# Optimization experiments

Measured on AMD Instinct MI355X. Metric: run time of the kernel, lower is better.

## Reference

```python
import jax, jax.numpy as jnp
import numpy as np

B, S, H, L, NH, FF, V, NL = 16, 512, 768, 12, 12, 3072, 30522, 9
DH = H // NH


def setup_inputs() -> dict:
    key = jax.random.key(0)
    ks = iter(jax.random.split(key, 16))
    def w(shape, scale=0.02):
        return jax.random.normal(next(ks), shape, jnp.float32) * scale
    return {
        "input_word_ids": jax.random.randint(next(ks), (B, S), 0, V, jnp.int32),
        "input_mask": jnp.ones((B, S), jnp.int32),
        "input_type_ids": jnp.zeros((B, S), jnp.int32),
        "valid_mask": jax.random.randint(next(ks), (B, S), 0, 2, jnp.int32),
        "word_emb": w((V, H)),
        "pos_emb": w((S, H)),
        "type_emb": w((2, H)),
        "emb_ln_g": jnp.ones((H,), jnp.float32),
        "emb_ln_b": jnp.zeros((H,), jnp.float32),
        "Wq": w((L, H, H)), "bq": jnp.zeros((L, H), jnp.float32),
        "Wk": w((L, H, H)), "bk": jnp.zeros((L, H), jnp.float32),
        "Wv": w((L, H, H)), "bv": jnp.zeros((L, H), jnp.float32),
        "Wo": w((L, H, H)), "bo": jnp.zeros((L, H), jnp.float32),
        "ln1_g": jnp.ones((L, H), jnp.float32), "ln1_b": jnp.zeros((L, H), jnp.float32),
        "W1": w((L, H, FF)), "b1": jnp.zeros((L, FF), jnp.float32),
        "W2": w((L, FF, H)), "b2": jnp.zeros((L, H), jnp.float32),
        "ln2_g": jnp.ones((L, H), jnp.float32), "ln2_b": jnp.zeros((L, H), jnp.float32),
        "cls_W": w((H, NL)), "cls_b": jnp.zeros((NL,), jnp.float32),
    }


def _layer_norm(x, g, b):
    m = x.mean(-1, keepdims=True)
    v = ((x - m) ** 2).mean(-1, keepdims=True)
    return (x - m) * jax.lax.rsqrt(v + 1e-12) * g + b


def reference(input_word_ids, input_mask, input_type_ids, valid_mask,
              word_emb, pos_emb, type_emb, emb_ln_g, emb_ln_b,
              Wq, bq, Wk, bk, Wv, bv, Wo, bo, ln1_g, ln1_b,
              W1, b1, W2, b2, ln2_g, ln2_b, cls_W, cls_b):
    b, s = input_word_ids.shape
    # --- BERT embeddings ---
    x = word_emb[input_word_ids] + pos_emb[None, :s] + type_emb[input_type_ids]
    x = _layer_norm(x, emb_ln_g, emb_ln_b)  # [B,S,H]
    attn_bias = (1.0 - input_mask.astype(jnp.float32))[:, None, None, :] * -1e9
    scale = 1.0 / np.sqrt(DH).astype(np.float32)

    def step(h, p):
        wq, bq_, wk, bk_, wv, bv_, wo, bo_, g1, gb1, w1, wb1, w2, wb2, g2, gb2 = p
        q = (h @ wq + bq_).reshape(b, s, NH, DH)
        k = (h @ wk + bk_).reshape(b, s, NH, DH)
        v = (h @ wv + bv_).reshape(b, s, NH, DH)
        scores = jnp.einsum('bqhd,bkhd->bhqk', q, k) * scale + attn_bias
        probs = jax.nn.softmax(scores, axis=-1)
        ctx = jnp.einsum('bhqk,bkhd->bqhd', probs, v).reshape(b, s, H)
        h = _layer_norm(h + ctx @ wo + bo_, g1, gb1)
        ff = jax.nn.gelu(h @ w1 + wb1, approximate=False)
        h = _layer_norm(h + ff @ w2 + wb2, g2, gb2)
        return h, None

    params = (Wq, bq, Wk, bk, Wv, bv, Wo, bo, ln1_g, ln1_b, W1, b1, W2, b2, ln2_g, ln2_b)
    x, _ = jax.lax.scan(step, x, params)

    # --- valid-token compaction (vectorized form of the python double loop) ---
    # valid tokens packed to the front (stable order), remainder zero-padded
    invalid = (1 - valid_mask).astype(jnp.int32)
    perm = jnp.argsort(invalid, axis=1, stable=True)          # [B,S]
    compact = jnp.take_along_axis(x, perm[:, :, None], axis=1)
    counts = valid_mask.sum(axis=1)                           # [B]
    keep = (jnp.arange(s)[None, :] < counts[:, None])[:, :, None]
    compact = jnp.where(keep, compact, jnp.zeros((), x.dtype))
    # dropout is identity at inference (training=False)
    logits = jax.nn.softmax(compact @ cls_W + cls_b, axis=-1)  # [B,S,NL]
    return logits
```

## Files before the change

### kernel.cpp

```cpp
#include <hip/hip_runtime.h>
#include <cstdint>
#include <cstddef>

#define B_ 16
#define S_ 512
#define H_ 768
#define L_ 12
#define NH_ 12
#define DH_ 64
#define FF_ 3072
#define NL_ 9
#define QKV_ 2304

typedef _Float16 f16x8 __attribute__((ext_vector_type(8)));
typedef float f32x4 __attribute__((ext_vector_type(4)));

__device__ __forceinline__ void load_lds16(const void* g, void* l) {
  __builtin_amdgcn_global_load_lds(
      (const __attribute__((address_space(1))) unsigned int*)g,
      (__attribute__((address_space(3))) unsigned int*)l, 16, 0, 0);
}

__device__ __forceinline__ float block_sum256(float v, float* red) {
#pragma unroll
  for (int off = 32; off; off >>= 1) v += __shfl_down(v, off);
  __syncthreads();
  if ((threadIdx.x & 63) == 0) red[threadIdx.x >> 6] = v;
  __syncthreads();
  return red[0] + red[1] + red[2] + red[3];
}

__device__ __forceinline__ float gelu_f(float x) {
  return 0.5f * x * (1.0f + erff(x * 0.70710678118654752f));
}

__global__ __launch_bounds__(256) void embed_ln_kernel(
    const int* __restrict__ wid, const int* __restrict__ tpid,
    const float* __restrict__ we, const float* __restrict__ pe,
    const float* __restrict__ te, const float* __restrict__ g,
    const float* __restrict__ bb, float* __restrict__ h,
    _Float16* __restrict__ hb) {
  __shared__ float red[4];
  int tok = blockIdx.x;
  int s = tok & (S_ - 1);
  int w = wid[tok], tp = tpid[tok];
  int t = threadIdx.x;
  float x[3];
#pragma unroll
  for (int i = 0; i < 3; ++i) {
    int j = t + i * 256;
    x[i] = we[(size_t)w * H_ + j] + pe[(size_t)s * H_ + j] + te[(size_t)tp * H_ + j];
  }
  float m = block_sum256(x[0] + x[1] + x[2], red) * (1.0f / H_);
  float d0 = x[0] - m, d1 = x[1] - m, d2 = x[2] - m;
  float var = block_sum256(d0 * d0 + d1 * d1 + d2 * d2, red) * (1.0f / H_);
  float rs = rsqrtf(var + 1e-12f);
#pragma unroll
  for (int i = 0; i < 3; ++i) {
    int j = t + i * 256;
    float v = (x[i] - m) * rs * g[j] + bb[j];
    h[(size_t)tok * H_ + j] = v;
    hb[(size_t)tok * H_ + j] = (_Float16)v;
  }
}

__global__ __launch_bounds__(256) void add_ln_kernel(
    float* __restrict__ h, const float* __restrict__ delta,
    const float* __restrict__ g, const float* __restrict__ bb,
    _Float16* __restrict__ hb) {
  __shared__ float red[4];
  int tok = blockIdx.x;
  int t = threadIdx.x;
  float x[3];
#pragma unroll
  for (int i = 0; i < 3; ++i) {
    int j = t + i * 256;
    x[i] = h[(size_t)tok * H_ + j] + delta[(size_t)tok * H_ + j];
  }
  float m = block_sum256(x[0] + x[1] + x[2], red) * (1.0f / H_);
  float d0 = x[0] - m, d1 = x[1] - m, d2 = x[2] - m;
  float var = block_sum256(d0 * d0 + d1 * d1 + d2 * d2, red) * (1.0f / H_);
  float rs = rsqrtf(var + 1e-12f);
#pragma unroll
  for (int i = 0; i < 3; ++i) {
    int j = t + i * 256;
    float v = (x[i] - m) * rs * g[j] + bb[j];
    h[(size_t)tok * H_ + j] = v;
    hb[(size_t)tok * H_ + j] = (_Float16)v;
  }
}

__global__ __launch_bounds__(256) void convert_weights_kernel(
    const float* __restrict__ Wq, const float* __restrict__ Wk,
    const float* __restrict__ Wv, const float* __restrict__ Wo,
    const float* __restrict__ W1, const float* __restrict__ W2,
    _Float16* __restrict__ qT, _Float16* __restrict__ kT,
    _Float16* __restrict__ vT, _Float16* __restrict__ oT,
    _Float16* __restrict__ w1T, _Float16* __restrict__ w2T,
    const float* __restrict__ bq, const float* __restrict__ bk,
    const float* __restrict__ bv, float* __restrict__ qkvb) {
  int id = blockIdx.x;
  int tid = threadIdx.x;
  if (id == 1728) {
    for (int j = tid; j < H_; j += 256) {
      qkvb[j] = bq[j];
      qkvb[H_ + j] = bk[j];
      qkvb[2 * H_ + j] = bv[j];
    }
    return;
  }
  __shared__ float T[64][65];
  const float* src;
  _Float16* dst;
  int K, N, tk, tn;
  if (id < 576) {
    int mat = id / 144, t = id % 144;
    K = 768; N = 768; tk = t / 12; tn = t % 12;
    src = (mat == 0) ? Wq : (mat == 1) ? Wk : (mat == 2) ? Wv : Wo;
    dst = (mat == 0) ? qT : (mat == 1) ? kT : (mat == 2) ? vT : oT;
  } else if (id < 1152) {
    int t = id - 576; K = 768; N = 3072; tk = t / 48; tn = t % 48;
    src = W1; dst = w1T;
  } else {
    int t = id - 1152; K = 3072; N = 768; tk = t / 12; tn = t % 12;
    src = W2; dst = w2T;
  }
  int k0 = tk * 64, n0 = tn * 64;
  {
    int r = tid >> 4, c4 = (tid & 15) * 4;
#pragma unroll
    for (int i = 0; i < 4; ++i) {
      float4 v = *(const float4*)&src[(size_t)(k0 + r + i * 16) * N + n0 + c4];
      T[r + i * 16][c4 + 0] = v.x;
      T[r + i * 16][c4 + 1] = v.y;
      T[r + i * 16][c4 + 2] = v.z;
      T[r + i * 16][c4 + 3] = v.w;
    }
  }
  __syncthreads();
#pragma unroll
  for (int i = 0; i < 2; ++i) {
    int chunk = tid + i * 256;
    int n = chunk >> 3, kc = (chunk & 7) * 8;
    f16x8 o;
#pragma unroll
    for (int j = 0; j < 8; ++j) o[j] = (_Float16)T[kc + j][n];
    *(f16x8*)&dst[(size_t)(n0 + n) * K + k0 + kc] = o;
  }
}

template <int OUT>
__global__ __launch_bounds__(256) void gemm_f16(
    const _Float16* __restrict__ A, const _Float16* __restrict__ Bt,
    const float* __restrict__ bias, void* __restrict__ Cv,
    int M, int N, int K) {
  __shared__ _Float16 As[2][128 * 32];
  __shared__ _Float16 Bs[2][128 * 32];
  int tid = threadIdx.x;
  int lane = tid & 63, w = tid >> 6;
  int wr = w >> 1, wc = w & 1;
  int l15 = lane & 15, kb = lane >> 4;
  int swk = (l15 >> 1) & 3;

  int nwg = gridDim.x * gridDim.y;
  int bid = blockIdx.y * gridDim.x + blockIdx.x;
  int swz = bid;
  if ((nwg & 7) == 0) {
    int cpx = nwg >> 3;
    swz = (bid & 7) * cpx + (bid >> 3);
  }
  int bx = swz % gridDim.x, by = swz / gridDim.x;
  int row0 = by * 128, col0 = bx * 128;

  int srow = lane >> 2;
  int schunk = (lane & 3) ^ ((lane >> 3) & 3);
  int scol = schunk * 8;
  const _Float16* gA0 = A + (size_t)(row0 + (w * 2 + 0) * 16 + srow) * K + scol;
  const _Float16* gA1 = A + (size_t)(row0 + (w * 2 + 1) * 16 + srow) * K + scol;
  const _Float16* gB0 = Bt + (size_t)(col0 + (w * 2 + 0) * 16 + srow) * K + scol;
  const _Float16* gB1 = Bt + (size_t)(col0 + (w * 2 + 1) * 16 + srow) * K + scol;
  int o0 = (w * 2 + 0) * 1024;
  int o1 = (w * 2 + 1) * 1024;

  f32x4 acc[4][4] = {};
  int nk = K >> 5;

  load_lds16(gA0, (char*)&As[0][0] + o0);
  load_lds16(gA1, (char*)&As[0][0] + o1);
  load_lds16(gB0, (char*)&Bs[0][0] + o0);
  load_lds16(gB1, (char*)&Bs[0][0] + o1);
  __syncthreads();

  for (int kt = 0; kt < nk; ++kt) {
    int cur = kt & 1;
    if (kt + 1 < nk) {
      int ko = (kt + 1) * 32;
      load_lds16(gA0 + ko, (char*)&As[cur ^ 1][0] + o0);
      load_lds16(gA1 + ko, (char*)&As[cur ^ 1][0] + o1);
      load_lds16(gB0 + ko, (char*)&Bs[cur ^ 1][0] + o0);
      load_lds16(gB1 + ko, (char*)&Bs[cur ^ 1][0] + o1);
    }
    f16x8 af[4], bf[4];
    int rpos = (kb ^ swk) * 8;
#pragma unroll
    for (int m = 0; m < 4; ++m)
      af[m] = *(const f16x8*)&As[cur][(wr * 64 + m * 16 + l15) * 32 + rpos];
#pragma unroll
    for (int n = 0; n < 4; ++n)
      bf[n] = *(const f16x8*)&Bs[cur][(wc * 64 + n * 16 + l15) * 32 + rpos];
#pragma unroll
    for (int m = 0; m < 4; ++m)
#pragma unroll
      for (int n = 0; n < 4; ++n)
        acc[m][n] = __builtin_amdgcn_mfma_f32_16x16x32_f16(af[m], bf[n], acc[m][n], 0, 0, 0);
    __syncthreads();
  }
#pragma unroll
  for (int n = 0; n < 4; ++n) {
    int col = col0 + wc * 64 + n * 16 + l15;
    float bv = bias[col];
#pragma unroll
    for (int m = 0; m < 4; ++m) {
      int rowb = row0 + wr * 64 + m * 16 + kb * 4;
#pragma unroll
      for (int r = 0; r < 4; ++r) {
        float v = acc[m][n][r] + bv;
        if (OUT == 2) v = gelu_f(v);
        if (OUT == 0)
          ((float*)Cv)[(size_t)(rowb + r) * N + col] = v;
        else
          ((_Float16*)Cv)[(size_t)(rowb + r) * N + col] = (_Float16)v;
      }
    }
  }
}

__global__ __launch_bounds__(256) void vtrans_kernel(
    const _Float16* __restrict__ v, int RS, _Float16* __restrict__ vt) {
  __shared__ _Float16 T[64][72];
  int s0 = blockIdx.x * 64;
  int bh = blockIdx.y;
  int b = bh / NH_, h = bh % NH_;
  int tid = threadIdx.x;
#pragma unroll
  for (int i = 0; i < 2; ++i) {
    int chunk = tid + i * 256;
    int s = chunk >> 3, dc = (chunk & 7) * 8;
    *(f16x8*)&T[s][dc] = *(const f16x8*)&v[(size_t)(b * S_ + s0 + s) * RS + h * DH_ + dc];
  }
  __syncthreads();
#pragma unroll
  for (int i = 0; i < 2; ++i) {
    int chunk = tid + i * 256;
    int d = chunk >> 3, sc = (chunk & 7) * 8;
    f16x8 o;
#pragma unroll
    for (int j = 0; j < 8; ++j) o[j] = T[sc + j][d];
    *(f16x8*)&vt[(size_t)(bh * DH_ + d) * S_ + s0 + sc] = o;
  }
}

__global__ __launch_bounds__(256) void flash_attn_kernel(
    const _Float16* __restrict__ q, const _Float16* __restrict__ k,
    const _Float16* __restrict__ vt, int RS, const int* __restrict__ mask,
    _Float16* __restrict__ ctx) {
  __shared__ _Float16 Ks[128 * 72];
  __shared__ _Float16 Vs[64 * 136];
  __shared__ _Float16 Ps[4][16 * 136];
  __shared__ float biasz[S_];
  int qt = blockIdx.x, h = blockIdx.y, b = blockIdx.z;
  int tid = threadIdx.x, lane = tid & 63, w = tid >> 6;
  int l15 = lane & 15, kb = lane >> 4;
  const float C = 0.125f * 1.44269504088896f;

  for (int i = tid; i < S_; i += 256)
    biasz[i] = (1.0f - (float)mask[b * S_ + i]) * (-1e9f * C);

  int qrow = b * S_ + qt * 64 + w * 16 + l15;
  f16x8 qf[2];
  qf[0] = *(const f16x8*)&q[(size_t)qrow * RS + h * DH_ + kb * 8];
  qf[1] = *(const f16x8*)&q[(size_t)qrow * RS + h * DH_ + 32 + kb * 8];

  auto loadKV = [&](int kt, f16x8* rk, f16x8* rv) {
#pragma unroll
    for (int i = 0; i < 4; ++i) {
      int idx = tid + i * 256;
      int r = idx >> 3, c = idx & 7;
      rk[i] = *(const f16x8*)&k[(size_t)(b * S_ + kt * 128 + r) * RS + h * DH_ + c * 8];
      int d = idx >> 4, c2 = idx & 15;
      rv[i] = *(const f16x8*)&vt[(size_t)((b * NH_ + h) * DH_ + d) * S_ + kt * 128 + c2 * 8];
    }
  };

  float m_run[4], l_run[4];
  f32x4 o[4] = {};
#pragma unroll
  for (int r = 0; r < 4; ++r) { m_run[r] = -1e30f; l_run[r] = 0.f; }

  f16x8 rk[4], rv[4];
  loadKV(0, rk, rv);
  for (int kt = 0; kt < 4; ++kt) {
    __syncthreads();
#pragma unroll
    for (int i = 0; i < 4; ++i) {
      int idx = tid + i * 256;
      int r = idx >> 3, c = idx & 7;
      *(f16x8*)&Ks[r * 72 + c * 8] = rk[i];
      int d = idx >> 4, c2 = idx & 15;
      *(f16x8*)&Vs[d * 136 + c2 * 8] = rv[i];
    }
    __syncthreads();
    if (kt < 3) loadKV(kt + 1, rk, rv);
    f32x4 s[8];
#pragma unroll
    for (int nf = 0; nf < 8; ++nf) {
      f16x8 b0 = *(const f16x8*)&Ks[(nf * 16 + l15) * 72 + kb * 8];
      f16x8 b1 = *(const f16x8*)&Ks[(nf * 16 + l15) * 72 + 32 + kb * 8];
      f32x4 z = {};
      z = __builtin_amdgcn_mfma_f32_16x16x32_f16(qf[0], b0, z, 0, 0, 0);
      z = __builtin_amdgcn_mfma_f32_16x16x32_f16(qf[1], b1, z, 0, 0, 0);
      s[nf] = z;
    }
    float zb[8];
#pragma unroll
    for (int nf = 0; nf < 8; ++nf) zb[nf] = biasz[kt * 128 + nf * 16 + l15];
    float pw[8][4];
    float corr[4];
#pragma unroll
    for (int r = 0; r < 4; ++r) {
      float mx = -1e30f;
#pragma unroll
      for (int nf = 0; nf < 8; ++nf) mx = fmaxf(mx, s[nf][r] * C + zb[nf]);
#pragma unroll
      for (int d = 1; d < 16; d <<= 1) mx = fmaxf(mx, __shfl_xor(mx, d));
      float mnew = fmaxf(m_run[r], mx);
      float cr = exp2f(m_run[r] - mnew);
      m_run[r] = mnew;
      corr[r] = cr;
      float sum = 0.f;
#pragma unroll
      for (int nf = 0; nf < 8; ++nf) {
        float pv = exp2f(s[nf][r] * C + zb[nf] - mnew);
        pw[nf][r] = pv;
        sum += pv;
      }
#pragma unroll
      for (int d = 1; d < 16; d <<= 1) sum += __shfl_xor(sum, d);
      l_run[r] = l_run[r] * cr + sum;
    }
#pragma unroll
    for (int nf2 = 0; nf2 < 4; ++nf2)
#pragma unroll
      for (int r = 0; r < 4; ++r) o[nf2][r] *= corr[r];
#pragma unroll
    for (int nf = 0; nf < 8; ++nf)
#pragma unroll
      for (int r = 0; r < 4; ++r)
        Ps[w][(kb * 4 + r) * 136 + nf * 16 + l15] = (_Float16)pw[nf][r];
#pragma unroll
    for (int ks = 0; ks < 4; ++ks) {
      f16x8 pa = *(const f16x8*)&Ps[w][l15 * 136 + ks * 32 + kb * 8];
#pragma unroll
      for (int nf2 = 0; nf2 < 4; ++nf2) {
        f16x8 vb2 = *(const f16x8*)&Vs[(nf2 * 16 + l15) * 136 + ks * 32 + kb * 8];
        o[nf2] = __builtin_amdgcn_mfma_f32_16x16x32_f16(pa, vb2, o[nf2], 0, 0, 0);
      }
    }
  }
  float inv[4];
#pragma unroll
  for (int r = 0; r < 4; ++r) inv[r] = 1.0f / fmaxf(l_run[r], 1e-37f);
#pragma unroll
  for (int nf2 = 0; nf2 < 4; ++nf2)
#pragma unroll
    for (int r = 0; r < 4; ++r) {
      int row = b * S_ + qt * 64 + w * 16 + kb * 4 + r;
      ctx[(size_t)row * H_ + h * DH_ + nf2 * 16 + l15] = (_Float16)(o[nf2][r] * inv[r]);
    }
}

__global__ void compact_idx_kernel(const int* __restrict__ valid, int* __restrict__ dest) {
  int b = threadIdx.x;
  if (b >= B_) return;
  int cnt = 0;
  for (int s = 0; s < S_; ++s) {
    int vv = valid[b * S_ + s];
    dest[b * S_ + s] = vv ? cnt : -1;
    cnt += vv;
  }
}

__global__ __launch_bounds__(256) void scatter_kernel(
    const float* __restrict__ h, const int* __restrict__ dest,
    float* __restrict__ compact) {
  int tok = blockIdx.x;
  int d = dest[tok];
  if (d < 0) return;
  int b = tok >> 9;
  size_t src = (size_t)tok * H_;
  size_t dst = ((size_t)(b * S_ + d)) * H_;
  for (int j = threadIdx.x; j < H_; j += 256) compact[dst + j] = h[src + j];
}

__global__ __launch_bounds__(256) void cls_kernel(
    const float* __restrict__ x, const float* __restrict__ W,
    const float* __restrict__ bias2, float* __restrict__ out) {
  int lane = threadIdx.x & 63, wv = threadIdx.x >> 6;
  int tok = blockIdx.x * 4 + wv;
  float acc[NL_] = {};
  for (int hh = lane; hh < H_; hh += 64) {
    float xv = x[(size_t)tok * H_ + hh];
#pragma unroll
    for (int n = 0; n < NL_; ++n) acc[n] = fmaf(xv, W[hh * NL_ + n], acc[n]);
  }
#pragma unroll
  for (int n = 0; n < NL_; ++n) {
#pragma unroll
    for (int off = 32; off; off >>= 1) acc[n] += __shfl_down(acc[n], off);
  }
  if (lane == 0) {
    float vls[NL_], mx = -1e30f;
#pragma unroll
    for (int n = 0; n < NL_; ++n) {
      vls[n] = acc[n] + bias2[n];
      mx = fmaxf(mx, vls[n]);
    }
    float s = 0.f;
#pragma unroll
    for (int n = 0; n < NL_; ++n) {
      vls[n] = expf(vls[n] - mx);
      s += vls[n];
    }
    float inv = 1.0f / s;
#pragma unroll
    for (int n = 0; n < NL_; ++n) out[(size_t)tok * NL_ + n] = vls[n] * inv;
  }
}

extern "C" void kernel_launch(void* const* d_in, const int* in_sizes, int n_in,
                              void* d_out, int out_size, void* d_ws, size_t ws_size,
                              hipStream_t stream) {
  const int* wid = (const int*)d_in[0];
  const int* mask = (const int*)d_in[1];
  const int* tpid = (const int*)d_in[2];
  const int* valid = (const int*)d_in[3];
  const float* we = (const float*)d_in[4];
  const float* pe = (const float*)d_in[5];
  const float* te = (const float*)d_in[6];
  const float* eg = (const float*)d_in[7];
  const float* eb = (const float*)d_in[8];
  const float* Wq = (const float*)d_in[9];
  const float* bq = (const float*)d_in[10];
  const float* Wk = (const float*)d_in[11];
  const float* bk = (const float*)d_in[12];
  const float* Wv = (const float*)d_in[13];
  const float* bv = (const float*)d_in[14];
  const float* Wo = (const float*)d_in[15];
  const float* bo = (const float*)d_in[16];
  const float* g1 = (const float*)d_in[17];
  const float* gb1 = (const float*)d_in[18];
  const float* W1 = (const float*)d_in[19];
  const float* bf1 = (const float*)d_in[20];
  const float* W2 = (const float*)d_in[21];
  const float* bf2 = (const float*)d_in[22];
  const float* g2 = (const float*)d_in[23];
  const float* gb2 = (const float*)d_in[24];
  const float* cW = (const float*)d_in[25];
  const float* cb = (const float*)d_in[26];
  float* out = (float*)d_out;

  const size_t TOK = (size_t)B_ * S_;
  char* ws = (char*)d_ws;
  float* h = (float*)ws;
  _Float16* hb = (_Float16*)(ws + 25165824);
  float* t1 = (float*)(ws + 37748736);
  char* un1 = ws + 62914560;
  _Float16* qkv = (_Float16*)un1;
  _Float16* vt = (_Float16*)(un1 + 37748736);
  _Float16* ffh = (_Float16*)un1;
  _Float16* ctx = (_Float16*)(ws + 113246208);
  char* wbuf = ws + 125829120;
  _Float16* wqT = (_Float16*)wbuf;
  _Float16* wkT = (_Float16*)(wbuf + 1179648);
  _Float16* wvT = (_Float16*)(wbuf + 2359296);
  _Float16* woT = (_Float16*)(wbuf + 3538944);
  _Float16* w1T = (_Float16*)(wbuf + 4718592);
  _Float16* w2T = (_Float16*)(wbuf + 9437184);
  int* dest = (int*)(ws + 139984896);
  float* qkvb = (float*)(ws + 140017664);

  dim3 blk(256);
  embed_ln_kernel<<<dim3((unsigned)TOK), blk, 0, stream>>>(wid, tpid, we, pe, te, eg, eb, h, hb);

  dim3 gQKV(QKV_ / 128, TOK / 128);
  dim3 gH(H_ / 128, TOK / 128);
  dim3 gF(FF_ / 128, TOK / 128);
  for (int l = 0; l < L_; ++l) {
    convert_weights_kernel<<<dim3(1729), blk, 0, stream>>>(
        Wq + (size_t)l * H_ * H_, Wk + (size_t)l * H_ * H_,
        Wv + (size_t)l * H_ * H_, Wo + (size_t)l * H_ * H_,
        W1 + (size_t)l * H_ * FF_, W2 + (size_t)l * FF_ * H_,
        wqT, wkT, wvT, woT, w1T, w2T,
        bq + l * H_, bk + l * H_, bv + l * H_, qkvb);
    gemm_f16<1><<<gQKV, blk, 0, stream>>>(hb, wqT, qkvb, qkv, (int)TOK, QKV_, H_);
    vtrans_kernel<<<dim3(S_ / 64, B_ * NH_), blk, 0, stream>>>(qkv + 2 * H_, QKV_, vt);
    flash_attn_kernel<<<dim3(S_ / 64, NH_, B_), blk, 0, stream>>>(
        qkv, qkv + H_, vt, QKV_, mask, ctx);
    gemm_f16<0><<<gH, blk, 0, stream>>>(ctx, woT, bo + l * H_, t1, (int)TOK, H_, H_);
    add_ln_kernel<<<dim3((unsigned)TOK), blk, 0, stream>>>(h, t1, g1 + l * H_, gb1 + l * H_, hb);
    gemm_f16<2><<<gF, blk, 0, stream>>>(hb, w1T, bf1 + l * FF_, ffh, (int)TOK, FF_, H_);
    gemm_f16<0><<<gH, blk, 0, stream>>>(ffh, w2T, bf2 + l * H_, t1, (int)TOK, H_, FF_);
    add_ln_kernel<<<dim3((unsigned)TOK), blk, 0, stream>>>(h, t1, g2 + l * H_, gb2 + l * H_, hb);
  }

  compact_idx_kernel<<<1, 64, 0, stream>>>(valid, dest);
  hipMemsetAsync(t1, 0, TOK * H_ * sizeof(float), stream);
  scatter_kernel<<<dim3((unsigned)TOK), blk, 0, stream>>>(h, dest, t1);
  cls_kernel<<<dim3((unsigned)(TOK / 4)), blk, 0, stream>>>(t1, cW, cb, out);
}
```

Before: 3.644 ms.

## Triple-buffer GEMM LDS tiles with two-deep prefetch and explicit vmcnt waits

The f16 GEMM moves from double to triple buffering in LDS. Each iteration prefetches the tile two steps ahead and uses explicit s_waitcnt vmcnt counts plus raw barriers, so it waits only for the tile it is about to use. This gives global loads more time to land before the MFMA work needs them. In exchange, LDS use per block grows by half, which can lower occupancy, and correctness now depends on the hand-written wait counts matching the four loads issued per stage.

```diff
diff --git a/kernel.cpp b/kernel.cpp
--- a/kernel.cpp
+++ b/kernel.cpp
@@ -154,8 +154,8 @@
     const _Float16* __restrict__ A, const _Float16* __restrict__ Bt,
     const float* __restrict__ bias, void* __restrict__ Cv,
     int M, int N, int K) {
-  __shared__ _Float16 As[2][128 * 32];
-  __shared__ _Float16 Bs[2][128 * 32];
+  __shared__ _Float16 As[3][128 * 32];
+  __shared__ _Float16 Bs[3][128 * 32];
   int tid = threadIdx.x;
   int lane = tid & 63, w = tid >> 6;
   int wr = w >> 1, wc = w & 1;
@@ -182,38 +182,51 @@
   int o0 = (w * 2 + 0) * 1024;
   int o1 = (w * 2 + 1) * 1024;
 
+  auto STAGE = [&](int t, int buf) {
+    int ko = t * 32;
+    load_lds16(gA0 + ko, (char*)&As[buf][0] + o0);
+    load_lds16(gA1 + ko, (char*)&As[buf][0] + o1);
+    load_lds16(gB0 + ko, (char*)&Bs[buf][0] + o0);
+    load_lds16(gB1 + ko, (char*)&Bs[buf][0] + o1);
+  };
+
   f32x4 acc[4][4] = {};
   int nk = K >> 5;
 
-  load_lds16(gA0, (char*)&As[0][0] + o0);
-  load_lds16(gA1, (char*)&As[0][0] + o1);
-  load_lds16(gB0, (char*)&Bs[0][0] + o0);
-  load_lds16(gB1, (char*)&Bs[0][0] + o1);
-  __syncthreads();
-
-  for (int kt = 0; kt < nk; ++kt) {
-    int cur = kt & 1;
-    if (kt + 1 < nk) {
-      int ko = (kt + 1) * 32;
-      load_lds16(gA0 + ko, (char*)&As[cur ^ 1][0] + o0);
-      load_lds16(gA1 + ko, (char*)&As[cur ^ 1][0] + o1);
-      load_lds16(gB0 + ko, (char*)&Bs[cur ^ 1][0] + o0);
-      load_lds16(gB1 + ko, (char*)&Bs[cur ^ 1][0] + o1);
-    }
+  STAGE(0, 0);
+  STAGE(1, 1);
+  asm volatile("s_waitcnt vmcnt(4)" ::: "memory");
+  __builtin_amdgcn_s_barrier();
+  __builtin_amdgcn_sched_barrier(0);
+
+  for (int t = 0; t < nk; ++t) {
+    int buf = t % 3;
+    if (t + 2 < nk) {
+      STAGE(t + 2, (t + 2) % 3);
+      asm volatile("s_waitcnt vmcnt(8)" ::: "memory");
+    } else if (t + 1 < nk) {
+      asm volatile("s_waitcnt vmcnt(4)" ::: "memory");
+    } else {
+      asm volatile("s_waitcnt vmcnt(0)" ::: "memory");
+    }
+    __builtin_amdgcn_s_barrier();
+    __builtin_amdgcn_sched_barrier(0);
     f16x8 af[4], bf[4];
     int rpos = (kb ^ swk) * 8;
 #pragma unroll
     for (int m = 0; m < 4; ++m)
-      af[m] = *(const f16x8*)&As[cur][(wr * 64 + m * 16 + l15) * 32 + rpos];
+      af[m] = *(const f16x8*)&As[buf][(wr * 64 + m * 16 + l15) * 32 + rpos];
 #pragma unroll
     for (int n = 0; n < 4; ++n)
-      bf[n] = *(const f16x8*)&Bs[cur][(wc * 64 + n * 16 + l15) * 32 + rpos];
+      bf[n] = *(const f16x8*)&Bs[buf][(wc * 64 + n * 16 + l15) * 32 + rpos];
 #pragma unroll
     for (int m = 0; m < 4; ++m)
 #pragma unroll
       for (int n = 0; n < 4; ++n)
         acc[m][n] = __builtin_amdgcn_mfma_f32_16x16x32_f16(af[m], bf[n], acc[m][n], 0, 0, 0);
-    __syncthreads();
+    asm volatile("s_waitcnt lgkmcnt(0)" ::: "memory");
+    __builtin_amdgcn_sched_barrier(0);
+    __builtin_amdgcn_s_barrier();
   }
 #pragma unroll
   for (int n = 0; n < 4; ++n) {
```

Result: no change. 3.693 ms (+1.4%).

## Keep residual stream in fp16, fuse residual add into GEMM epilogue, cheaper GELU

Applied to the files above, without the earlier changes.

Drops the fp32 residual copy of the hidden state. The residual add moves into the Wo and W2 GEMM epilogues, which now read the fp16 hidden state and write fp16 output. The add+LayerNorm kernels become fp16-input LayerNorm kernels with vectorized 192-thread blocks, and the final scatter reads fp16. erff in GELU is replaced by the Abramowitz-Stegun polynomial with __expf. This cuts fp32 memory traffic and epilogue math, at the cost of accuracy because the residual is accumulated in fp16 and GELU is approximated.

```diff
diff --git a/kernel.cpp b/kernel.cpp
--- a/kernel.cpp
+++ b/kernel.cpp
@@ -13,6 +13,7 @@
 #define QKV_ 2304
 
 typedef _Float16 f16x8 __attribute__((ext_vector_type(8)));
+typedef _Float16 f16x4 __attribute__((ext_vector_type(4)));
 typedef float f32x4 __attribute__((ext_vector_type(4)));
 
 __device__ __forceinline__ void load_lds16(const void* g, void* l) {
@@ -30,16 +31,30 @@
   return red[0] + red[1] + red[2] + red[3];
 }
 
+__device__ __forceinline__ float block_sum192(float v, float* red) {
+#pragma unroll
+  for (int off = 32; off; off >>= 1) v += __shfl_down(v, off);
+  __syncthreads();
+  if ((threadIdx.x & 63) == 0) red[threadIdx.x >> 6] = v;
+  __syncthreads();
+  return red[0] + red[1] + red[2];
+}
+
 __device__ __forceinline__ float gelu_f(float x) {
-  return 0.5f * x * (1.0f + erff(x * 0.70710678118654752f));
+  float au = fabsf(x) * 0.70710678118654752f;
+  float t = 1.0f / (1.0f + 0.3275911f * au);
+  float p = ((((1.061405429f * t - 1.453152027f) * t + 1.421413741f) * t
+              - 0.284496736f) * t + 0.254829592f) * t;
+  float e = p * __expf(-au * au);
+  float phi = (x >= 0.0f) ? (1.0f - 0.5f * e) : (0.5f * e);
+  return x * phi;
 }
 
 __global__ __launch_bounds__(256) void embed_ln_kernel(
     const int* __restrict__ wid, const int* __restrict__ tpid,
     const float* __restrict__ we, const float* __restrict__ pe,
     const float* __restrict__ te, const float* __restrict__ g,
-    const float* __restrict__ bb, float* __restrict__ h,
-    _Float16* __restrict__ hb) {
+    const float* __restrict__ bb, _Float16* __restrict__ hb) {
   __shared__ float red[4];
   int tok = blockIdx.x;
   int s = tok & (S_ - 1);
@@ -59,35 +74,32 @@
   for (int i = 0; i < 3; ++i) {
     int j = t + i * 256;
     float v = (x[i] - m) * rs * g[j] + bb[j];
-    h[(size_t)tok * H_ + j] = v;
     hb[(size_t)tok * H_ + j] = (_Float16)v;
   }
 }
 
-__global__ __launch_bounds__(256) void add_ln_kernel(
-    float* __restrict__ h, const float* __restrict__ delta,
-    const float* __restrict__ g, const float* __restrict__ bb,
-    _Float16* __restrict__ hb) {
-  __shared__ float red[4];
+__global__ __launch_bounds__(192) void ln_f16_kernel(
+    const _Float16* __restrict__ x, const float* __restrict__ g,
+    const float* __restrict__ bb, _Float16* __restrict__ hb) {
+  __shared__ float red[3];
   int tok = blockIdx.x;
   int t = threadIdx.x;
-  float x[3];
-#pragma unroll
-  for (int i = 0; i < 3; ++i) {
-    int j = t + i * 256;
-    x[i] = h[(size_t)tok * H_ + j] + delta[(size_t)tok * H_ + j];
-  }
-  float m = block_sum256(x[0] + x[1] + x[2], red) * (1.0f / H_);
-  float d0 = x[0] - m, d1 = x[1] - m, d2 = x[2] - m;
-  float var = block_sum256(d0 * d0 + d1 * d1 + d2 * d2, red) * (1.0f / H_);
+  int j = t * 4;
+  f16x4 xv = *(const f16x4*)&x[(size_t)tok * H_ + j];
+  float v0 = (float)xv[0], v1 = (float)xv[1], v2 = (float)xv[2], v3 = (float)xv[3];
+  float m = block_sum192(v0 + v1 + v2 + v3, red) * (1.0f / H_);
+  float d0 = v0 - m, d1 = v1 - m, d2 = v2 - m, d3 = v3 - m;
+  __syncthreads();
+  float var = block_sum192(d0 * d0 + d1 * d1 + d2 * d2 + d3 * d3, red) * (1.0f / H_);
   float rs = rsqrtf(var + 1e-12f);
-#pragma unroll
-  for (int i = 0; i < 3; ++i) {
-    int j = t + i * 256;
-    float v = (x[i] - m) * rs * g[j] + bb[j];
-    h[(size_t)tok * H_ + j] = v;
-    hb[(size_t)tok * H_ + j] = (_Float16)v;
-  }
+  float4 gv = *(const float4*)&g[j];
+  float4 bv = *(const float4*)&bb[j];
+  f16x4 o;
+  o[0] = (_Float16)(d0 * rs * gv.x + bv.x);
+  o[1] = (_Float16)(d1 * rs * gv.y + bv.y);
+  o[2] = (_Float16)(d2 * rs * gv.z + bv.z);
+  o[3] = (_Float16)(d3 * rs * gv.w + bv.w);
+  *(f16x4*)&hb[(size_t)tok * H_ + j] = o;
 }
 
 __global__ __launch_bounds__(256) void convert_weights_kernel(
@@ -153,7 +165,7 @@
 __global__ __launch_bounds__(256) void gemm_f16(
     const _Float16* __restrict__ A, const _Float16* __restrict__ Bt,
     const float* __restrict__ bias, void* __restrict__ Cv,
-    int M, int N, int K) {
+    int M, int N, int K, const _Float16* __restrict__ hres) {
   __shared__ _Float16 As[2][128 * 32];
   __shared__ _Float16 Bs[2][128 * 32];
   int tid = threadIdx.x;
@@ -226,10 +238,8 @@
       for (int r = 0; r < 4; ++r) {
         float v = acc[m][n][r] + bv;
         if (OUT == 2) v = gelu_f(v);
-        if (OUT == 0)
-          ((float*)Cv)[(size_t)(rowb + r) * N + col] = v;
-        else
-          ((_Float16*)Cv)[(size_t)(rowb + r) * N + col] = (_Float16)v;
+        if (OUT == 3) v += (float)hres[(size_t)(rowb + r) * N + col];
+        ((_Float16*)Cv)[(size_t)(rowb + r) * N + col] = (_Float16)v;
       }
     }
   }
@@ -390,16 +400,17 @@
   }
 }
 
-__global__ __launch_bounds__(256) void scatter_kernel(
-    const float* __restrict__ h, const int* __restrict__ dest,
+__global__ __launch_bounds__(192) void scatter_kernel(
+    const _Float16* __restrict__ hb, const int* __restrict__ dest,
     float* __restrict__ compact) {
   int tok = blockIdx.x;
   int d = dest[tok];
   if (d < 0) return;
   int b = tok >> 9;
-  size_t src = (size_t)tok * H_;
-  size_t dst = ((size_t)(b * S_ + d)) * H_;
-  for (int j = threadIdx.x; j < H_; j += 256) compact[dst + j] = h[src + j];
+  int j = threadIdx.x * 4;
+  f16x4 v = *(const f16x4*)&hb[(size_t)tok * H_ + j];
+  float4 o = {(float)v[0], (float)v[1], (float)v[2], (float)v[3]};
+  *(float4*)&compact[((size_t)(b * S_ + d)) * H_ + j] = o;
 }
 
 __global__ __launch_bounds__(256) void cls_kernel(
@@ -471,13 +482,13 @@
 
   const size_t TOK = (size_t)B_ * S_;
   char* ws = (char*)d_ws;
-  float* h = (float*)ws;
   _Float16* hb = (_Float16*)(ws + 25165824);
-  float* t1 = (float*)(ws + 37748736);
+  _Float16* t1h = (_Float16*)(ws + 37748736);
   char* un1 = ws + 62914560;
   _Float16* qkv = (_Float16*)un1;
   _Float16* vt = (_Float16*)(un1 + 37748736);
   _Float16* ffh = (_Float16*)un1;
+  float* compactf = (float*)un1;
   _Float16* ctx = (_Float16*)(ws + 113246208);
   char* wbuf = ws + 125829120;
   _Float16* wqT = (_Float16*)wbuf;
@@ -490,7 +501,8 @@
   float* qkvb = (float*)(ws + 140017664);
 
   dim3 blk(256);
-  embed_ln_kernel<<<dim3((unsigned)TOK), blk, 0, stream>>>(wid, tpid, we, pe, te, eg, eb, h, hb);
+  dim3 blk192(192);
+  embed_ln_kernel<<<dim3((unsigned)TOK), blk, 0, stream>>>(wid, tpid, we, pe, te, eg, eb, hb);
 
   dim3 gQKV(QKV_ / 128, TOK / 128);
   dim3 gH(H_ / 128, TOK / 128);
@@ -502,19 +514,19 @@
         W1 + (size_t)l * H_ * FF_, W2 + (size_t)l * FF_ * H_,
         wqT, wkT, wvT, woT, w1T, w2T,
         bq + l * H_, bk + l * H_, bv + l * H_, qkvb);
-    gemm_f16<1><<<gQKV, blk, 0, stream>>>(hb, wqT, qkvb, qkv, (int)TOK, QKV_, H_);
+    gemm_f16<1><<<gQKV, blk, 0, stream>>>(hb, wqT, qkvb, qkv, (int)TOK, QKV_, H_, nullptr);
     vtrans_kernel<<<dim3(S_ / 64, B_ * NH_), blk, 0, stream>>>(qkv + 2 * H_, QKV_, vt);
     flash_attn_kernel<<<dim3(S_ / 64, NH_, B_), blk, 0, stream>>>(
         qkv, qkv + H_, vt, QKV_, mask, ctx);
-    gemm_f16<0><<<gH, blk, 0, stream>>>(ctx, woT, bo + l * H_, t1, (int)TOK, H_, H_);
-    add_ln_kernel<<<dim3((unsigned)TOK), blk, 0, stream>>>(h, t1, g1 + l * H_, gb1 + l * H_, hb);
-    gemm_f16<2><<<gF, blk, 0, stream>>>(hb, w1T, bf1 + l * FF_, ffh, (int)TOK, FF_, H_);
-    gemm_f16<0><<<gH, blk, 0, stream>>>(ffh, w2T, bf2 + l * H_, t1, (int)TOK, H_, FF_);
-    add_ln_kernel<<<dim3((unsigned)TOK), blk, 0, stream>>>(h, t1, g2 + l * H_, gb2 + l * H_, hb);
+    gemm_f16<3><<<gH, blk, 0, stream>>>(ctx, woT, bo + l * H_, t1h, (int)TOK, H_, H_, hb);
+    ln_f16_kernel<<<dim3((unsigned)TOK), blk192, 0, stream>>>(t1h, g1 + l * H_, gb1 + l * H_, hb);
+    gemm_f16<2><<<gF, blk, 0, stream>>>(hb, w1T, bf1 + l * FF_, ffh, (int)TOK, FF_, H_, nullptr);
+    gemm_f16<3><<<gH, blk, 0, stream>>>(ffh, w2T, bf2 + l * H_, t1h, (int)TOK, H_, FF_, hb);
+    ln_f16_kernel<<<dim3((unsigned)TOK), blk192, 0, stream>>>(t1h, g2 + l * H_, gb2 + l * H_, hb);
   }
 
   compact_idx_kernel<<<1, 64, 0, stream>>>(valid, dest);
-  hipMemsetAsync(t1, 0, TOK * H_ * sizeof(float), stream);
-  scatter_kernel<<<dim3((unsigned)TOK), blk, 0, stream>>>(h, dest, t1);
-  cls_kernel<<<dim3((unsigned)(TOK / 4)), blk, 0, stream>>>(t1, cW, cb, out);
-}
+  hipMemsetAsync(compactf, 0, TOK * H_ * sizeof(float), stream);
+  scatter_kernel<<<dim3((unsigned)TOK), blk192, 0, stream>>>(hb, dest, compactf);
+  cls_kernel<<<dim3((unsigned)(TOK / 4)), blk, 0, stream>>>(compactf, cW, cb, out);
+}
```

Result: no change. 3.661 ms (+0.5%).
